# Performance work log

Measured on AMD Instinct MI355X. Metric: run time of the kernel, lower is better.

The kernel has to match this reference:

```python
import jax, jax.numpy as jnp
import numpy as np

N = 100000        # n_nodes (entities)
B = 1024          # batch of users
S = 32            # edge_threshold (sampled edges per node)
M = 64            # adj_matrix neighbors per node
D_IN = 64         # in_channel[0]
HID = 32          # out_channel[0] == in_channel[1]
D_OUT = 64        # out_channel[1]
K_STEP = 2
NUM_SAMPLE = 32
ITEM_LO, ITEM_HI = 0, 39999
SLOPE = 0.01      # leaky_relu default negative slope


def setup_inputs() -> dict:
    key = jax.random.key(0)
    ks = jax.random.split(key, 12)
    sc = lambda *sh: 1.0 / np.sqrt(sh[-1])
    return {
        "entity_embedding": jax.random.normal(ks[0], (N, D_IN), jnp.float32) * 0.1,
        "W1l": jax.random.normal(ks[1], (HID, D_IN), jnp.float32) * sc(HID, D_IN),
        "W1r": jax.random.normal(ks[2], (HID, D_IN), jnp.float32) * sc(HID, D_IN),
        "b1": jnp.zeros((HID,), jnp.float32),
        "W2l": jax.random.normal(ks[3], (D_OUT, HID), jnp.float32) * sc(D_OUT, HID),
        "W2r": jax.random.normal(ks[4], (D_OUT, HID), jnp.float32) * sc(D_OUT, HID),
        "b2": jnp.zeros((D_OUT,), jnp.float32),
        "disc_emb": jax.random.normal(ks[5], (N, D_OUT), jnp.float32) * 0.1,
        "users": jax.random.randint(ks[6], (B,), 0, ITEM_HI + 1, jnp.int32),
        "pos": jax.random.randint(ks[7], (B,), 0, ITEM_HI + 1, jnp.int32),
        "adj_matrix": jax.random.randint(ks[8], (N, M), 0, N, jnp.int32),
        "edge_matrix": jax.random.randint(ks[9], (N, S), 0, N, jnp.int32),
    }


def _leaky(x):
    return jnp.where(x >= 0, x, SLOPE * x)


def _sage(x, src, dst, Wl, Wr, b):
    # PyG SAGEConv: lin_l(mean_{j->i} x_j) + lin_r(x_i)
    sums = jax.ops.segment_sum(x[src], dst, num_segments=N)
    cnt = jax.ops.segment_sum(jnp.ones(src.shape, x.dtype), dst, num_segments=N)
    mean = sums / jnp.maximum(cnt, 1.0)[:, None]
    return mean @ Wl.T + b + x @ Wr.T


def _gcn(x, src, dst, W1l, W1r, b1, W2l, W2r, b2):
    h = _leaky(_sage(x, src, dst, W1l, W1r, b1))   # dropout = identity (eval)
    h = _sage(h, src, dst, W2l, W2r, b2)
    nrm = jnp.sqrt(jnp.sum(h * h, axis=1, keepdims=True))
    return h / jnp.maximum(nrm, 1e-12)             # F.normalize


def _kg_step(gcn, pos_idx, users, adj, explore_flag, step):
    u_e = gcn[users]                               # [B, d]
    pos_e = gcn[pos_idx]                           # [B, d]
    one_hop = adj[pos_idx] if explore_flag == 1 else adj[users]   # [B, M]
    i_e = gcn[one_hop]                             # [B, M, d]
    p = jnp.einsum('bmd,bd->bm', _leaky(pos_e[:, None, :] * i_e), u_e)
    logits = jax.nn.softmax(p, axis=1)
    if step == 1:
        nid = jnp.argmax(logits, axis=1)[:, None]
    else:
        _, nid = jax.lax.top_k(logits, NUM_SAMPLE)
    cand = jnp.take_along_axis(one_hop, nid, axis=1)
    prob = jnp.log(jnp.take_along_axis(logits, nid, axis=1))
    if step == 1:
        return cand[:, 0], prob[:, 0]
    return cand, prob


def _filter_entity(cand, key):
    rnd = jax.random.randint(key, cand.shape, ITEM_LO, ITEM_HI + 1, dtype=cand.dtype)
    bad = (cand > ITEM_HI) | (cand < ITEM_LO)
    return jnp.where(bad, rnd, cand)


def _prune_step(disc_emb, users, pos2, negs, logits):
    # stand-in for discriminator.item_rank (no_grad in original)
    u = jax.lax.stop_gradient(disc_emb[users])
    ranking = jnp.einsum('bd,bjd->bj', u,
                         jax.lax.stop_gradient(disc_emb[pos2] - disc_emb[negs]))
    idx = jnp.argmin(ranking, axis=1)[:, None]
    good_neg = jnp.take_along_axis(negs, idx, axis=1)[:, 0]
    good_logits = jnp.take_along_axis(logits, idx, axis=1)[:, 0]
    return good_neg, good_logits


def reference(entity_embedding, W1l, W1r, b1, W2l, W2r, b2, disc_emb,
              users, pos, adj_matrix, edge_matrix):
    src = jnp.repeat(jnp.arange(N, dtype=jnp.int32), S)   # build_edge node_index
    dst = edge_matrix.reshape(-1)
    gcn = _gcn(entity_embedding, src, dst, W1l, W1r, b1, W2l, W2r, b2)
    fkey = jax.random.key(123)
    neg_list, prob_list = [], []
    p = pos
    for k in range(K_STEP):
        one_hop, one_hop_logits = _kg_step(gcn, p, users, adj_matrix, 1, 1)
        cand, two_logits = _kg_step(gcn, one_hop, users, adj_matrix, 1, 2)
        cand = _filter_entity(cand, jax.random.fold_in(fkey, 2 * k))
        pos2, _ = _kg_step(gcn, p, users, adj_matrix, 2, 2)
        pos2 = _filter_entity(pos2, jax.random.fold_in(fkey, 2 * k + 1))
        good_neg, good_logits = _prune_step(disc_emb, users, pos2, cand, two_logits)
        good_logits = good_logits + one_hop_logits
        neg_list.append(good_neg)
        prob_list.append(good_logits)
        p = good_neg
    return jnp.stack(neg_list), jnp.stack(prob_list)
```

## Files before the change

### kernel.cpp

```cpp
#include <hip/hip_runtime.h>
#include <hip/hip_bf16.h>

#define N_NODES 100000
#define N_EDGES (N_NODES * 32)
#define BATCH   1024
#define SPAN    40000u
#define MULT    7296u
#define FILL_B  (N_EDGES / 256)

#define NB_BKT 391
#define EPB    4096
#define SBLK   782
#define BKT_CAP 8960


__host__ __device__ inline void threefry2x32(unsigned k0, unsigned k1,
                                             unsigned x0, unsigned x1,
                                             unsigned* o0, unsigned* o1)
{
  unsigned ks2 = k0 ^ k1 ^ 0x1BD11BDAu;
  unsigned v0 = x0 + k0, v1 = x1 + k1;
#define RL(x,d) (((x) << (d)) | ((x) >> (32 - (d))))
#define G4(a,b,c,dd) \
  v0 += v1; v1 = RL(v1,a);  v1 ^= v0; \
  v0 += v1; v1 = RL(v1,b);  v1 ^= v0; \
  v0 += v1; v1 = RL(v1,c);  v1 ^= v0; \
  v0 += v1; v1 = RL(v1,dd); v1 ^= v0;
  G4(13,15,26,6)  v0 += k1;  v1 += ks2 + 1u;
  G4(17,29,16,24) v0 += ks2; v1 += k0 + 2u;
  G4(13,15,26,6)  v0 += k0;  v1 += k1 + 3u;
  G4(17,29,16,24) v0 += k1;  v1 += ks2 + 4u;
  G4(13,15,26,6)  v0 += ks2; v1 += k0 + 5u;
#undef G4
#undef RL
  *o0 = v0; *o1 = v1;
}

__device__ __forceinline__ float bcastf(float v, int l)
{
  return __int_as_float(__builtin_amdgcn_readlane(__float_as_int(v), l));
}


__global__ void k_init_buckets(int* __restrict__ bbase, int* __restrict__ bcur)
{
  int i = blockIdx.x * 256 + threadIdx.x;
  if (i < NB_BKT) { bbase[i] = i * BKT_CAP; bcur[i] = i * BKT_CAP; }
}

__global__ __launch_bounds__(256) void k_bucket_hist(
    const int* __restrict__ edge, int* __restrict__ bhist)
{
  __shared__ int h[NB_BKT];
  for (int i = threadIdx.x; i < NB_BKT; i += 256) h[i] = 0;
  __syncthreads();
  int base = blockIdx.x * EPB;
  int cnt = N_EDGES - base; if (cnt > EPB) cnt = EPB;
  const int4* e4 = (const int4*)(edge + base);
  int nq = cnt >> 2;
  for (int i = threadIdx.x; i < nq; i += 256) {
    int4 v = e4[i];
    atomicAdd(&h[v.x >> 8], 1); atomicAdd(&h[v.y >> 8], 1);
    atomicAdd(&h[v.z >> 8], 1); atomicAdd(&h[v.w >> 8], 1);
  }
  __syncthreads();
  for (int i = threadIdx.x; i < NB_BKT; i += 256)
    if (h[i]) atomicAdd(&bhist[i], h[i]);
}

__global__ void k_scan_buckets(const int* __restrict__ bhist,
                               int* __restrict__ bbase, int* __restrict__ bcur)
{
  __shared__ int s[512];
  int t = threadIdx.x;
  s[t] = (t < NB_BKT) ? bhist[t] : 0;
  __syncthreads();
  for (int o = 1; o < 512; o <<= 1) {
    int u = (t >= o) ? s[t - o] : 0;
    __syncthreads();
    s[t] += u;
    __syncthreads();
  }
  if (t < NB_BKT) {
    int excl = s[t] - bhist[t];
    bbase[t] = excl;
    bcur[t]  = excl;
  }
}

__global__ __launch_bounds__(256) void k_bucket_scatter(
    const int* __restrict__ edge, int* __restrict__ bcur,
    int* __restrict__ pairs)
{
  __shared__ int  h[NB_BKT];
  __shared__ int  lbase[NB_BKT];
  __shared__ int  gbase[NB_BKT];
  __shared__ int  lcur[NB_BKT];
  __shared__ int2 buf[EPB];
  int t = threadIdx.x;
  for (int i = t; i < NB_BKT; i += 256) h[i] = 0;
  __syncthreads();
  int base = blockIdx.x * EPB;
  int cnt = N_EDGES - base; if (cnt > EPB) cnt = EPB;
  const int4* e4 = (const int4*)(edge + base);
  int nq = cnt >> 2;
  for (int i = t; i < nq; i += 256) {
    int4 v = e4[i];
    atomicAdd(&h[v.x >> 8], 1); atomicAdd(&h[v.y >> 8], 1);
    atomicAdd(&h[v.z >> 8], 1); atomicAdd(&h[v.w >> 8], 1);
  }
  __syncthreads();
  if (t < 64) {
    int run = 0;
    for (int c = 0; c < NB_BKT; c += 64) {
      int idx = c + t;
      int v = (idx < NB_BKT) ? h[idx] : 0;
      int orig = v;
      for (int o = 1; o < 64; o <<= 1) {
        int u = __shfl_up(v, o);
        if (t >= o) v += u;
      }
      if (idx < NB_BKT) lbase[idx] = run + v - orig;
      run += __shfl(v, 63);
    }
  }
  __syncthreads();
  for (int i = t; i < NB_BKT; i += 256) lcur[i] = lbase[i];
  __syncthreads();
  for (int i = t; i < nq; i += 256) {
    int4 v = e4[i];
    int eid = base + (i << 2);
    int p;
    p = atomicAdd(&lcur[v.x >> 8], 1); buf[p] = make_int2(v.x, (eid + 0) >> 5);
    p = atomicAdd(&lcur[v.y >> 8], 1); buf[p] = make_int2(v.y, (eid + 1) >> 5);
    p = atomicAdd(&lcur[v.z >> 8], 1); buf[p] = make_int2(v.z, (eid + 2) >> 5);
    p = atomicAdd(&lcur[v.w >> 8], 1); buf[p] = make_int2(v.w, (eid + 3) >> 5);
  }
  __syncthreads();
  for (int i = t; i < NB_BKT; i += 256) {
    int c = lcur[i] - lbase[i];
    gbase[i] = (c > 0) ? atomicAdd(&bcur[i], c) : 0;
  }
  __syncthreads();
  for (int i = t; i < cnt; i += 256) {
    int2 pr = buf[i];
    int b = pr.x >> 8;
    pairs[gbase[b] + (i - lbase[b])] = (pr.y << 8) | (pr.x & 255);
  }
}

__global__ __launch_bounds__(256) void k_bucket_csr(
    const int* __restrict__ bbase, const int* __restrict__ bcur,
    const int* __restrict__ pairs, int* __restrict__ csr,
    int* __restrict__ rowp, int* __restrict__ deg)
{
  __shared__ int nd[256], nb[256], nc[256];
  int b = blockIdx.x, t = threadIdx.x;
  int nb0 = b << 8;
  int ebase = bbase[b];
  int ecnt  = bcur[b] - ebase;
  nd[t] = 0; nc[t] = 0;
  __syncthreads();
  for (int i = t; i < ecnt; i += 256) {
    int pr = pairs[ebase + i];
    atomicAdd(&nd[pr & 255], 1);
  }
  __syncthreads();
  nb[t] = nd[t];
  __syncthreads();
  for (int o = 1; o < 256; o <<= 1) {
    int u = (t >= o) ? nb[t - o] : 0;
    __syncthreads();
    nb[t] += u;
    __syncthreads();
  }
  int excl = nb[t] - nd[t];
  int node = nb0 + t;
  if (node < N_NODES) { rowp[node] = ebase + excl; deg[node] = nd[t]; }
  __syncthreads();
  nb[t] = excl;
  __syncthreads();
  for (int i = t; i < ecnt; i += 256) {
    int pr = pairs[ebase + i];
    int l = pr & 255;
    int p = atomicAdd(&nc[l], 1);
    csr[ebase + nb[l] + p] = pr >> 8;
  }
}

__global__ __launch_bounds__(256) void k_gather_csr(
    const int* __restrict__ rowp, const int* __restrict__ deg,
    const int* __restrict__ csr, const float* __restrict__ src,
    float* __restrict__ out)
{
  int node = blockIdx.x * 8 + (threadIdx.x >> 5);
  int f = threadIdx.x & 31;
  int hb = threadIdx.x & 32;
  int sub = f >> 3;
  int q   = f & 7;
  int start = rowp[node];
  int dg = deg[node];
  const float4* src4 = (const float4*)src;
  float4 a0 = make_float4(0.f, 0.f, 0.f, 0.f);
  float4 a1 = make_float4(0.f, 0.f, 0.f, 0.f);
  for (int b0 = 0; b0 < dg; b0 += 32) {
    int idx = b0 + f;
    int e = (idx < dg) ? csr[start + idx] : -1;
#pragma unroll
    for (int j = 0; j < 8; j += 2) {
      int e0 = __shfl(e, hb + 4 * j + sub);
      int e1 = __shfl(e, hb + 4 * (j + 1) + sub);
      if (e0 >= 0) {
        float4 v = src4[(size_t)e0 * 8 + q];
        a0.x += v.x; a0.y += v.y; a0.z += v.z; a0.w += v.w;
      }
      if (e1 >= 0) {
        float4 v = src4[(size_t)e1 * 8 + q];
        a1.x += v.x; a1.y += v.y; a1.z += v.z; a1.w += v.w;
      }
    }
  }
  a0.x += a1.x; a0.y += a1.y; a0.z += a1.z; a0.w += a1.w;
  a0.x += __shfl_xor(a0.x, 8);  a0.y += __shfl_xor(a0.y, 8);
  a0.z += __shfl_xor(a0.z, 8);  a0.w += __shfl_xor(a0.w, 8);
  a0.x += __shfl_xor(a0.x, 16); a0.y += __shfl_xor(a0.y, 16);
  a0.z += __shfl_xor(a0.z, 16); a0.w += __shfl_xor(a0.w, 16);
  if (sub == 0) ((float4*)out)[(size_t)node * 8 + q] = a0;
}

__global__ __launch_bounds__(256) void k_fill_gemm(
    const int* __restrict__ edge, int* __restrict__ head, int* __restrict__ next,
    int nsub, const float* __restrict__ x, const float* __restrict__ W,
    float* __restrict__ y)
{
  __shared__ float sw[32 * 65];
  if (blockIdx.x < FILL_B) {
    int e = blockIdx.x * 256 + threadIdx.x;
    int d = edge[e];
    int sub = e & (nsub - 1);
    int old = atomicExch(head + sub * N_NODES + d, e);
    next[e] = old;
  } else {
    for (int t = threadIdx.x; t < 2048; t += 256) sw[(t >> 6) * 65 + (t & 63)] = W[t];
    __syncthreads();
    int i = (blockIdx.x - FILL_B) * 8 + (threadIdx.x >> 5);
    int f = threadIdx.x & 31;
    const float* xr = x + (size_t)i * 64;
    const float* wr = sw + f * 65;
    float acc = 0.f;
#pragma unroll
    for (int d = 0; d < 64; ++d) acc += xr[d] * wr[d];
    y[(size_t)i * 32 + f] = acc;
  }
}

template<int NSUB>
__global__ __launch_bounds__(256) void k_gather_ll(
    const int* __restrict__ head, const int* __restrict__ next,
    const float* __restrict__ src, float* __restrict__ out,
    int* __restrict__ deg_out)
{
  int node = blockIdx.x * 8 + (threadIdx.x >> 5);
  int f = threadIdx.x & 31;
  int hb = threadIdx.x & 32;
  int e = (f < NSUB) ? head[f * N_NODES + node] : -1;
  float acc = 0.f;
  int cnt = 0;
  while (true) {
    int es[NSUB];
    bool any = false;
#pragma unroll
    for (int j = 0; j < NSUB; ++j) { es[j] = __shfl(e, hb + j); any |= (es[j] != -1); }
    if (!any) break;
    int en = -1;
    if (f < NSUB && e != -1) en = next[e];
#pragma unroll
    for (int j = 0; j < NSUB; ++j)
      if (es[j] != -1) { acc += src[(size_t)(es[j] >> 5) * 32 + f]; cnt++; }
    e = en;
  }
  out[(size_t)node * 32 + f] = acc;
  if (deg_out != nullptr && f == 0) deg_out[node] = cnt;
}

#define DWB 1250
#define DNPW 20

__global__ __launch_bounds__(256) void k_gemm64x32(
    const float* __restrict__ x, const float* __restrict__ W, float* __restrict__ y)
{
  int lane = threadIdx.x & 63;
  int gw = blockIdx.x * 4 + (threadIdx.x >> 6);
  float wreg[64];
  const float* wrow = W + (size_t)(lane & 31) * 64;
#pragma unroll
  for (int d = 0; d < 64; ++d) wreg[d] = wrow[d];
  int n0 = gw * DNPW;
#pragma unroll 1
  for (int i = n0; i < n0 + DNPW; ++i) {
    float vin = x[(size_t)i * 64 + lane];
    float acc = 0.f;
#pragma unroll
    for (int d = 0; d < 64; ++d) acc += bcastf(vin, d) * wreg[d];
    if (lane < 32) y[(size_t)i * 32 + lane] = acc;
  }
}

__global__ __launch_bounds__(256) void k_scatter(
    const int* __restrict__ edge, const float* __restrict__ src,
    float* __restrict__ acc, int* __restrict__ cnt)
{
  int e = blockIdx.x * 8 + (threadIdx.x >> 5);
  int f = threadIdx.x & 31;
  int d = edge[e];
  atomicAdd(acc + (size_t)d * 32 + f, src[(size_t)(e >> 5) * 32 + f]);
  if (cnt != nullptr && f == 0) atomicAdd(cnt + d, 1);
}

__global__ __launch_bounds__(256) void k_layer1(
    const float* __restrict__ sum1, const int* __restrict__ cnt,
    const float* __restrict__ x, const float* __restrict__ W1r,
    const float* __restrict__ b1, float* __restrict__ h)
{
  int lane = threadIdx.x & 63;
  int gw = blockIdx.x * 4 + (threadIdx.x >> 6);
  float wreg[64];
  const float* wrow = W1r + (size_t)(lane & 31) * 64;
#pragma unroll
  for (int d = 0; d < 64; ++d) wreg[d] = wrow[d];
  float sb = b1[lane & 31];
  int n0 = gw * DNPW;
#pragma unroll 1
  for (int i = n0; i < n0 + DNPW; ++i) {
    float vin = x[(size_t)i * 64 + lane];
    float acc = 0.f;
#pragma unroll
    for (int d = 0; d < 64; ++d) acc += bcastf(vin, d) * wreg[d];
    if (lane < 32) {
      float c = fmaxf((float)cnt[i], 1.f);
      float mean = sum1[(size_t)i * 32 + lane] / c;
      float v = (mean + sb) + acc;
      h[(size_t)i * 32 + lane] = (v >= 0.f) ? v : 0.01f * v;
    }
  }
}

#define L2_BLOCKS 1250
#define L2_NPW    20
__global__ __launch_bounds__(256) void k_layer2(
    float* __restrict__ A, float* __restrict__ B, const int* __restrict__ cnt,
    const float* __restrict__ W2l, const float* __restrict__ W2r,
    const float* __restrict__ b2)
{
  int lane = threadIdx.x & 63;
  int gw = blockIdx.x * 4 + (threadIdx.x >> 6);
  float wl[32], wr[32];
#pragma unroll
  for (int f = 0; f < 32; ++f) { wl[f] = W2l[lane * 32 + f]; wr[f] = W2r[lane * 32 + f]; }
  float bb = b2[lane];
  int n0 = gw * L2_NPW;
#pragma unroll 1
  for (int i = n0; i < n0 + L2_NPW; ++i) {
    float c = fmaxf((float)cnt[i], 1.f);
    float vin;
    if (lane < 32) vin = B[(size_t)i * 32 + lane] / c;
    else           vin = A[(size_t)i * 32 + (lane - 32)];
    float acc = 0.f, acc2 = 0.f;
#pragma unroll
    for (int f = 0; f < 32; ++f) {
      acc  += bcastf(vin, f)      * wl[f];
      acc2 += bcastf(vin, 32 + f) * wr[f];
    }
    float t = (acc + bb) + acc2;
    float s = t * t;
#pragma unroll
    for (int o = 32; o > 0; o >>= 1) s += __shfl_xor(s, o);
    float g = t / fmaxf(sqrtf(s), 1e-12f);
    if (lane < 32) A[(size_t)i * 32 + lane]        = g;
    else           B[(size_t)i * 32 + (lane - 32)] = g;
  }
}


__device__ inline float kg_score_lds(const float* __restrict__ row,
                                     const float* sp, const float* su)
{
  float acc = 0.f;
#pragma unroll
  for (int d = 0; d < 64; ++d) {
    float t = sp[d] * row[d];
    t = (t >= 0.f) ? t : 0.01f * t;
    acc += t * su[d];
  }
  return acc;
}

__device__ inline float wave_softmax(float acc)
{
  float m = acc;
#pragma unroll
  for (int o = 32; o > 0; o >>= 1) m = fmaxf(m, __shfl_xor(m, o));
  float e = expf(acc - m);
  float Z = e;
#pragma unroll
  for (int o = 32; o > 0; o >>= 1) Z += __shfl_xor(Z, o);
  return e / Z;
}

__device__ inline void load_row(const float* glo, const float* ghi, int node,
                                int lane, float* smem)
{
  smem[lane] = (lane < 32) ? glo[(size_t)node * 32 + lane]
                           : ghi[(size_t)node * 32 + (lane - 32)];
}

__device__ inline void stage_rows(const float* __restrict__ glo,
                                  const float* __restrict__ ghi,
                                  int nb, int lane, float* sn)
{
#pragma unroll
  for (int j = 0; j < 64; ++j) {
    int rj = __builtin_amdgcn_readlane(nb, j);
    float v = (lane < 32) ? glo[(size_t)rj * 32 + lane]
                          : ghi[(size_t)rj * 32 + (lane - 32)];
    sn[j * 65 + lane] = v;
  }
}

__global__ __launch_bounds__(64) void k_kg_argmax(
    const float* __restrict__ glo, const float* __restrict__ ghi,
    const int* __restrict__ users, const int* __restrict__ pvec,
    const int* __restrict__ adj, int* __restrict__ sel_out,
    float* __restrict__ logit_out)
{
  int b = blockIdx.x, lane = threadIdx.x;
  int u = users[b], pb = pvec[b];
  __shared__ float su[64], sp[64];
  __shared__ float sn[64 * 65];
  load_row(glo, ghi, u,  lane, su);
  load_row(glo, ghi, pb, lane, sp);
  int nb = adj[(size_t)pb * 64 + lane];
  stage_rows(glo, ghi, nb, lane, sn);
  __syncthreads();
  float sm = wave_softmax(kg_score_lds(sn + lane * 65, sp, su));
  float v = sm; int i = lane;
#pragma unroll
  for (int o = 32; o > 0; o >>= 1) {
    float ov = __shfl_xor(v, o); int oi = __shfl_xor(i, o);
    if (ov > v || (ov == v && oi < i)) { v = ov; i = oi; }
  }
  float smw = __shfl(sm, i);
  int sel = __shfl(nb, i);
  if (lane == 0) { sel_out[b] = sel; logit_out[b] = logf(smw); }
}

__global__ __launch_bounds__(64) void k_kg_topk2(
    const float* __restrict__ glo, const float* __restrict__ ghi,
    const int* __restrict__ users, const int* __restrict__ srcA,
    const int* __restrict__ pvecB, const int* __restrict__ adj,
    unsigned a1a, unsigned a1b, unsigned a2a, unsigned a2b,
    unsigned c1a, unsigned c1b, unsigned c2a, unsigned c2b,
    int* __restrict__ candA, float* __restrict__ logA, int* __restrict__ candB)
{
  int b = blockIdx.x & (BATCH - 1);
  int var = blockIdx.x >> 10;
  int lane = threadIdx.x;
  int u = users[b];
  int pidx = (var == 0) ? srcA[b] : pvecB[b];
  int nbr  = (var == 0) ? srcA[b] : u;
  unsigned k1a = (var == 0) ? a1a : c1a, k1b = (var == 0) ? a1b : c1b;
  unsigned k2a = (var == 0) ? a2a : c2a, k2b = (var == 0) ? a2b : c2b;
  int* cand_out = (var == 0) ? candA : candB;
  float* logit_out = (var == 0) ? logA : nullptr;

  __shared__ float su[64], sp[64];
  __shared__ float sn[64 * 65];
  load_row(glo, ghi, u,    lane, su);
  load_row(glo, ghi, pidx, lane, sp);
  int nb = adj[(size_t)nbr * 64 + lane];
  stage_rows(glo, ghi, nb, lane, sn);
  __syncthreads();
  float sm = wave_softmax(kg_score_lds(sn + lane * 65, sp, su));
  int r = 0;
#pragma unroll
  for (int j = 0; j < 64; ++j) {
    float sj = bcastf(sm, j);
    if (sj > sm || (sj == sm && j < lane)) ++r;
  }
  if (r < 32) {
    int cand = nb;
    if (logit_out != nullptr) logit_out[b * 32 + r] = logf(sm);
    unsigned j = (unsigned)(b * 32 + r);
    unsigned h0, h1, l0, l1;
    threefry2x32(k1a, k1b, 0u, j, &h0, &h1);
    threefry2x32(k2a, k2b, 0u, j, &l0, &l1);
    unsigned hi = h0 ^ h1, lo = l0 ^ l1;
    unsigned rnd = ((hi % SPAN) * MULT + (lo % SPAN)) % SPAN;
    if (cand > 39999 || cand < 0) cand = (int)rnd;
    cand_out[b * 32 + r] = cand;
  }
}

__global__ __launch_bounds__(64) void k_kg_prune(
    const float* __restrict__ disc, const int* __restrict__ users,
    const int* __restrict__ cand, const float* __restrict__ two_log,
    const int* __restrict__ pos2, const float* __restrict__ one_log,
    float* __restrict__ out, int k, int* __restrict__ p_next)
{
  int b = blockIdx.x, lane = threadIdx.x;
  __shared__ float su[64];
  __shared__ float sd[64 * 65];
  su[lane] = disc[(size_t)users[b] * 64 + lane];
  int pr = (lane < 32) ? pos2[b * 32 + lane] : cand[b * 32 + (lane - 32)];
#pragma unroll
  for (int j = 0; j < 64; ++j) {
    int rj = __builtin_amdgcn_readlane(pr, j);
    sd[j * 65 + lane] = disc[(size_t)rj * 64 + lane];
  }
  __syncthreads();
  float r = 1e30f;
  if (lane < 32) {
    const float* dp = sd + lane * 65;
    const float* dn = sd + (32 + lane) * 65;
    float acc = 0.f;
#pragma unroll
    for (int d = 0; d < 64; ++d) acc += su[d] * (dp[d] - dn[d]);
    r = acc;
  }
  float v = r; int i = lane;
#pragma unroll
  for (int o = 32; o > 0; o >>= 1) {
    float ov = __shfl_xor(v, o); int oi = __shfl_xor(i, o);
    if (ov < v || (ov == v && oi < i)) { v = ov; i = oi; }
  }
  if (lane == 0) {
    int gn = cand[b * 32 + i];
    float gl = two_log[b * 32 + i] + one_log[b];
    out[k * BATCH + b]             = (float)gn;
    out[2 * BATCH + k * BATCH + b] = gl;
    p_next[b] = gn;
  }
}

extern "C" void kernel_launch(void* const* d_in, const int* in_sizes, int n_in,
                              void* d_out, int out_size, void* d_ws, size_t ws_size,
                              hipStream_t stream)
{
  const float* x    = (const float*)d_in[0];
  const float* W1l  = (const float*)d_in[1];
  const float* W1r  = (const float*)d_in[2];
  const float* b1   = (const float*)d_in[3];
  const float* W2l  = (const float*)d_in[4];
  const float* W2r  = (const float*)d_in[5];
  const float* b2   = (const float*)d_in[6];
  const float* disc = (const float*)d_in[7];
  const int*   users= (const int*)d_in[8];
  const int*   pos  = (const int*)d_in[9];
  const int*   adj  = (const int*)d_in[10];
  const int*   edge = (const int*)d_in[11];
  float* out = (float*)d_out;

  char* w = (char*)d_ws;
  const size_t NEED_FIX = 42036480;
  const size_t NEED_CSR = 39617792;
  float *A, *B;
  char* bb;

  if (ws_size >= NEED_FIX) {
    int*  csr   = (int*)(w);
    int*  rowp  = (int*)(w + 14013440);
    int*  deg   = (int*)(w + 14413440);
    int*  bbase = (int*)(w + 14813440);
    int*  bcur  = (int*)(w + 14815488);
    int*  pairs = (int*)(w + 14817536);
    A = (float*)(w + 14817536);
    B = (float*)(w + 28830976);
    bb = w + 41630976;
    k_init_buckets<<<2, 256, 0, stream>>>(bbase, bcur);
    k_bucket_scatter<<<SBLK, 256, 0, stream>>>(edge, bcur, pairs);
    k_bucket_csr<<<NB_BKT, 256, 0, stream>>>(bbase, bcur, pairs, csr, rowp, deg);
    k_gemm64x32<<<DWB, 256, 0, stream>>>(x, W1l, A);
    k_gather_csr<<<N_NODES / 8, 256, 0, stream>>>(rowp, deg, csr, A, B);
    k_layer1<<<DWB, 256, 0, stream>>>(B, deg, x, W1r, b1, A);
    k_gather_csr<<<N_NODES / 8, 256, 0, stream>>>(rowp, deg, csr, A, B);
    k_layer2<<<L2_BLOCKS, 256, 0, stream>>>(A, B, deg, W2l, W2r, b2);
  } else if (ws_size >= NEED_CSR) {
    int*  csr   = (int*)(w);
    int*  rowp  = (int*)(w + 12800000);
    int*  deg   = (int*)(w + 13200000);
    int*  bhist = (int*)(w + 13600000);
    int*  bbase = (int*)(w + 13604096);
    int*  bcur  = (int*)(w + 13608192);
    int*  pairs = (int*)(w + 13612288);
    A = (float*)(w + 13612288);
    B = (float*)(w + 26412288);
    bb = w + 39212288;
    hipMemsetAsync(bhist, 0, 4096, stream);
    k_bucket_hist<<<SBLK, 256, 0, stream>>>(edge, bhist);
    k_scan_buckets<<<1, 512, 0, stream>>>(bhist, bbase, bcur);
    k_bucket_scatter<<<SBLK, 256, 0, stream>>>(edge, bcur, pairs);
    k_bucket_csr<<<NB_BKT, 256, 0, stream>>>(bbase, bcur, pairs, csr, rowp, deg);
    k_gemm64x32<<<DWB, 256, 0, stream>>>(x, W1l, A);
    k_gather_csr<<<N_NODES / 8, 256, 0, stream>>>(rowp, deg, csr, A, B);
    k_layer1<<<DWB, 256, 0, stream>>>(B, deg, x, W1r, b1, A);
    k_gather_csr<<<N_NODES / 8, 256, 0, stream>>>(rowp, deg, csr, A, B);
    k_layer2<<<L2_BLOCKS, 256, 0, stream>>>(A, B, deg, W2l, W2r, b2);
  } else {
    int* cnt = (int*)w;
    A = (float*)(w + 409600);
    B = (float*)(w + 13209600);
    bb = w + 26009600;
    hipMemsetAsync(cnt, 0, 400000, stream);
    hipMemsetAsync(B, 0, 12800000, stream);
    k_gemm64x32<<<DWB, 256, 0, stream>>>(x, W1l, A);
    k_scatter<<<N_EDGES / 8, 256, 0, stream>>>(edge, A, B, cnt);
    k_layer1<<<DWB, 256, 0, stream>>>(B, cnt, x, W1r, b1, A);
    hipMemsetAsync(B, 0, 12800000, stream);
    k_scatter<<<N_EDGES / 8, 256, 0, stream>>>(edge, A, B, nullptr);
    k_layer2<<<L2_BLOCKS, 256, 0, stream>>>(A, B, cnt, W2l, W2r, b2);
  }

  int*   p_cur       = (int*)(bb);
  int*   one_hop_sel = (int*)(bb + 4096);
  float* one_hop_log = (float*)(bb + 8192);
  int*   cand        = (int*)(bb + 12288);
  float* two_log     = (float*)(bb + 143360);
  int*   pos2        = (int*)(bb + 274432);

  for (int k = 0; k < 2; ++k) {
    unsigned f0, f1, a1a, a1b, a2a, a2b, c1a, c1b, c2a, c2b;
    threefry2x32(0u, 123u, 0u, (unsigned)(2 * k), &f0, &f1);
    threefry2x32(f0, f1, 0u, 0u, &a1a, &a1b);
    threefry2x32(f0, f1, 0u, 1u, &a2a, &a2b);
    threefry2x32(0u, 123u, 0u, (unsigned)(2 * k + 1), &f0, &f1);
    threefry2x32(f0, f1, 0u, 0u, &c1a, &c1b);
    threefry2x32(f0, f1, 0u, 1u, &c2a, &c2b);

    const int* pvec = (k == 0) ? pos : p_cur;
    k_kg_argmax<<<BATCH, 64, 0, stream>>>(A, B, users, pvec, adj, one_hop_sel, one_hop_log);
    k_kg_topk2<<<2 * BATCH, 64, 0, stream>>>(A, B, users, one_hop_sel, pvec, adj,
                                             a1a, a1b, a2a, a2b, c1a, c1b, c2a, c2b,
                                             cand, two_log, pos2);
    k_kg_prune<<<BATCH, 64, 0, stream>>>(disc, users, cand, two_log, pos2,
                                         one_hop_log, out, k, p_cur);
  }
}
```

Before: 456.4 us.

## Remap dense GEMM kernels to one node per lane with uniform weight loads

Rewrites the three dense per-node transforms (W1l projection, layer1 and layer2) so each lane owns one node and accumulates all outputs in registers. Weights are read as wave-uniform float4 loads instead of readlane broadcasts, and the grid is sized to 391 blocks. The aim is to remove the readlane/broadcast overhead and the half-idle lanes of the old wave-per-node scheme. In exchange each lane reads its node row as strided float4 (uncoalesced across lanes) and register pressure rises; an asm barrier fixes the reduction order in layer2's norm.

```diff
diff --git a/kernel.cpp b/kernel.cpp
--- a/kernel.cpp
+++ b/kernel.cpp
@@ -41,6 +41,12 @@
   return __int_as_float(__builtin_amdgcn_readlane(__float_as_int(v), l));
 }
 
+__device__ __forceinline__ float fbar(float v)
+{
+  asm volatile("" : "+v"(v));
+  return v;
+}
+
 
 __global__ void k_init_buckets(int* __restrict__ bbase, int* __restrict__ bcur)
 {
@@ -283,26 +289,37 @@
   if (deg_out != nullptr && f == 0) deg_out[node] = cnt;
 }
 
-#define DWB 1250
-#define DNPW 20
-
-__global__ __launch_bounds__(256) void k_gemm64x32(
+#define DGB 391
+
+__global__ __launch_bounds__(256, 4) void k_gemm64x32(
     const float* __restrict__ x, const float* __restrict__ W, float* __restrict__ y)
 {
   int lane = threadIdx.x & 63;
-  int gw = blockIdx.x * 4 + (threadIdx.x >> 6);
-  float wreg[64];
-  const float* wrow = W + (size_t)(lane & 31) * 64;
-#pragma unroll
-  for (int d = 0; d < 64; ++d) wreg[d] = wrow[d];
-  int n0 = gw * DNPW;
+  int wv = blockIdx.x * 4 + (threadIdx.x >> 6);
+  int node = wv * 64 + lane;
+  bool ok = node < N_NODES;
+  const float4* x4 = (const float4*)(x + (size_t)node * 64);
+  const float4* W4 = (const float4*)W;
+  float acc[32];
+#pragma unroll
+  for (int o = 0; o < 32; ++o) acc[o] = 0.f;
 #pragma unroll 1
-  for (int i = n0; i < n0 + DNPW; ++i) {
-    float vin = x[(size_t)i * 64 + lane];
-    float acc = 0.f;
-#pragma unroll
-    for (int d = 0; d < 64; ++d) acc += bcastf(vin, d) * wreg[d];
-    if (lane < 32) y[(size_t)i * 32 + lane] = acc;
+  for (int j = 0; j < 16; ++j) {
+    float4 xv = ok ? x4[j] : make_float4(0.f, 0.f, 0.f, 0.f);
+#pragma unroll
+    for (int o = 0; o < 32; ++o) {
+      float4 wv4 = W4[o * 16 + j];
+      acc[o] += wv4.x * xv.x;
+      acc[o] += wv4.y * xv.y;
+      acc[o] += wv4.z * xv.z;
+      acc[o] += wv4.w * xv.w;
+    }
+  }
+  if (ok) {
+    float4* y4 = (float4*)(y + (size_t)node * 32);
+#pragma unroll
+    for (int k = 0; k < 8; ++k)
+      y4[k] = make_float4(acc[4 * k], acc[4 * k + 1], acc[4 * k + 2], acc[4 * k + 3]);
   }
 }
 
@@ -317,67 +334,141 @@
   if (cnt != nullptr && f == 0) atomicAdd(cnt + d, 1);
 }
 
-__global__ __launch_bounds__(256) void k_layer1(
+__global__ __launch_bounds__(256, 4) void k_layer1(
     const float* __restrict__ sum1, const int* __restrict__ cnt,
     const float* __restrict__ x, const float* __restrict__ W1r,
     const float* __restrict__ b1, float* __restrict__ h)
 {
   int lane = threadIdx.x & 63;
-  int gw = blockIdx.x * 4 + (threadIdx.x >> 6);
-  float wreg[64];
-  const float* wrow = W1r + (size_t)(lane & 31) * 64;
-#pragma unroll
-  for (int d = 0; d < 64; ++d) wreg[d] = wrow[d];
-  float sb = b1[lane & 31];
-  int n0 = gw * DNPW;
+  int wv = blockIdx.x * 4 + (threadIdx.x >> 6);
+  int node = wv * 64 + lane;
+  bool ok = node < N_NODES;
+  const float4* x4 = (const float4*)(x + (size_t)node * 64);
+  const float4* W4 = (const float4*)W1r;
+  float acc[32];
+#pragma unroll
+  for (int o = 0; o < 32; ++o) acc[o] = 0.f;
 #pragma unroll 1
-  for (int i = n0; i < n0 + DNPW; ++i) {
-    float vin = x[(size_t)i * 64 + lane];
-    float acc = 0.f;
-#pragma unroll
-    for (int d = 0; d < 64; ++d) acc += bcastf(vin, d) * wreg[d];
-    if (lane < 32) {
-      float c = fmaxf((float)cnt[i], 1.f);
-      float mean = sum1[(size_t)i * 32 + lane] / c;
-      float v = (mean + sb) + acc;
-      h[(size_t)i * 32 + lane] = (v >= 0.f) ? v : 0.01f * v;
+  for (int j = 0; j < 16; ++j) {
+    float4 xv = ok ? x4[j] : make_float4(0.f, 0.f, 0.f, 0.f);
+#pragma unroll
+    for (int o = 0; o < 32; ++o) {
+      float4 wv4 = W4[o * 16 + j];
+      acc[o] += wv4.x * xv.x;
+      acc[o] += wv4.y * xv.y;
+      acc[o] += wv4.z * xv.z;
+      acc[o] += wv4.w * xv.w;
     }
   }
-}
-
-#define L2_BLOCKS 1250
-#define L2_NPW    20
-__global__ __launch_bounds__(256) void k_layer2(
+  if (ok) {
+    float c = fmaxf((float)cnt[node], 1.f);
+    const float4* s4 = (const float4*)(sum1 + (size_t)node * 32);
+    float4* h4 = (float4*)(h + (size_t)node * 32);
+#pragma unroll
+    for (int k = 0; k < 8; ++k) {
+      float4 sv = s4[k];
+      float4 r;
+      r.x = ((sv.x / c) + b1[4 * k + 0]) + acc[4 * k + 0];
+      r.y = ((sv.y / c) + b1[4 * k + 1]) + acc[4 * k + 1];
+      r.z = ((sv.z / c) + b1[4 * k + 2]) + acc[4 * k + 2];
+      r.w = ((sv.w / c) + b1[4 * k + 3]) + acc[4 * k + 3];
+      r.x = (r.x >= 0.f) ? r.x : 0.01f * r.x;
+      r.y = (r.y >= 0.f) ? r.y : 0.01f * r.y;
+      r.z = (r.z >= 0.f) ? r.z : 0.01f * r.z;
+      r.w = (r.w >= 0.f) ? r.w : 0.01f * r.w;
+      h4[k] = r;
+    }
+  }
+}
+
+__device__ __forceinline__ void l2_half(
+    const float4* B4, const float4* A4, const float4* Wl4, const float4* Wr4,
+    const float* b2, float c, bool ok, int obase, float* t)
+{
+  float accA[32];
+#pragma unroll
+  for (int o = 0; o < 32; ++o) accA[o] = 0.f;
+#pragma unroll 1
+  for (int j = 0; j < 8; ++j) {
+    float4 bv = ok ? B4[j] : make_float4(0.f, 0.f, 0.f, 0.f);
+    bv.x /= c; bv.y /= c; bv.z /= c; bv.w /= c;
+#pragma unroll
+    for (int o = 0; o < 32; ++o) {
+      float4 w = Wl4[(obase + o) * 8 + j];
+      accA[o] += w.x * bv.x;
+      accA[o] += w.y * bv.y;
+      accA[o] += w.z * bv.z;
+      accA[o] += w.w * bv.w;
+    }
+  }
+#pragma unroll
+  for (int o = 0; o < 32; ++o) accA[o] = accA[o] + b2[obase + o];
+  float accB[32];
+#pragma unroll
+  for (int o = 0; o < 32; ++o) accB[o] = 0.f;
+#pragma unroll 1
+  for (int j = 0; j < 8; ++j) {
+    float4 av = ok ? A4[j] : make_float4(0.f, 0.f, 0.f, 0.f);
+#pragma unroll
+    for (int o = 0; o < 32; ++o) {
+      float4 w = Wr4[(obase + o) * 8 + j];
+      accB[o] += w.x * av.x;
+      accB[o] += w.y * av.y;
+      accB[o] += w.z * av.z;
+      accB[o] += w.w * av.w;
+    }
+  }
+#pragma unroll
+  for (int o = 0; o < 32; ++o) t[o] = accA[o] + accB[o];
+}
+
+__global__ __launch_bounds__(256, 4) void k_layer2(
     float* __restrict__ A, float* __restrict__ B, const int* __restrict__ cnt,
     const float* __restrict__ W2l, const float* __restrict__ W2r,
     const float* __restrict__ b2)
 {
   int lane = threadIdx.x & 63;
-  int gw = blockIdx.x * 4 + (threadIdx.x >> 6);
-  float wl[32], wr[32];
-#pragma unroll
-  for (int f = 0; f < 32; ++f) { wl[f] = W2l[lane * 32 + f]; wr[f] = W2r[lane * 32 + f]; }
-  float bb = b2[lane];
-  int n0 = gw * L2_NPW;
-#pragma unroll 1
-  for (int i = n0; i < n0 + L2_NPW; ++i) {
-    float c = fmaxf((float)cnt[i], 1.f);
-    float vin;
-    if (lane < 32) vin = B[(size_t)i * 32 + lane] / c;
-    else           vin = A[(size_t)i * 32 + (lane - 32)];
-    float acc = 0.f, acc2 = 0.f;
-#pragma unroll
-    for (int f = 0; f < 32; ++f) {
-      acc  += bcastf(vin, f)      * wl[f];
-      acc2 += bcastf(vin, 32 + f) * wr[f];
+  int wv = blockIdx.x * 4 + (threadIdx.x >> 6);
+  int node = wv * 64 + lane;
+  bool ok = node < N_NODES;
+  float c = 1.f;
+  if (ok) c = fmaxf((float)cnt[node], 1.f);
+  const float4* B4 = (const float4*)(B + (size_t)node * 32);
+  const float4* A4 = (const float4*)(A + (size_t)node * 32);
+  const float4* Wl4 = (const float4*)W2l;
+  const float4* Wr4 = (const float4*)W2r;
+  float t0[32], t1[32];
+  l2_half(B4, A4, Wl4, Wr4, b2, c, ok, 0,  t0);
+  l2_half(B4, A4, Wl4, Wr4, b2, c, ok, 32, t1);
+  float a[32];
+#pragma unroll
+  for (int k = 0; k < 32; ++k) {
+    float v0 = fbar(t0[k] * t0[k]);
+    float v1 = fbar(t1[k] * t1[k]);
+    a[k] = v0 + v1;
+  }
+  float bv[16];
+#pragma unroll
+  for (int k = 0; k < 16; ++k) bv[k] = a[k] + a[k + 16];
+  float cv[8];
+#pragma unroll
+  for (int k = 0; k < 8; ++k) cv[k] = bv[k] + bv[k + 8];
+  float dv[4];
+#pragma unroll
+  for (int k = 0; k < 4; ++k) dv[k] = cv[k] + cv[k + 4];
+  float ev0 = dv[0] + dv[2], ev1 = dv[1] + dv[3];
+  float s = (ev0 + ev1);
+  float den = fmaxf(sqrtf(s), 1e-12f);
+  if (ok) {
+    float4* Ao = (float4*)(A + (size_t)node * 32);
+    float4* Bo = (float4*)(B + (size_t)node * 32);
+#pragma unroll
+    for (int k = 0; k < 8; ++k) {
+      Ao[k] = make_float4(t0[4 * k] / den, t0[4 * k + 1] / den,
+                          t0[4 * k + 2] / den, t0[4 * k + 3] / den);
+      Bo[k] = make_float4(t1[4 * k] / den, t1[4 * k + 1] / den,
+                          t1[4 * k + 2] / den, t1[4 * k + 3] / den);
     }
-    float t = (acc + bb) + acc2;
-    float s = t * t;
-#pragma unroll
-    for (int o = 32; o > 0; o >>= 1) s += __shfl_xor(s, o);
-    float g = t / fmaxf(sqrtf(s), 1e-12f);
-    if (lane < 32) A[(size_t)i * 32 + lane]        = g;
-    else           B[(size_t)i * 32 + (lane - 32)] = g;
   }
 }
 
@@ -579,11 +670,11 @@
     k_init_buckets<<<2, 256, 0, stream>>>(bbase, bcur);
     k_bucket_scatter<<<SBLK, 256, 0, stream>>>(edge, bcur, pairs);
     k_bucket_csr<<<NB_BKT, 256, 0, stream>>>(bbase, bcur, pairs, csr, rowp, deg);
-    k_gemm64x32<<<DWB, 256, 0, stream>>>(x, W1l, A);
+    k_gemm64x32<<<DGB, 256, 0, stream>>>(x, W1l, A);
     k_gather_csr<<<N_NODES / 8, 256, 0, stream>>>(rowp, deg, csr, A, B);
-    k_layer1<<<DWB, 256, 0, stream>>>(B, deg, x, W1r, b1, A);
+    k_layer1<<<DGB, 256, 0, stream>>>(B, deg, x, W1r, b1, A);
     k_gather_csr<<<N_NODES / 8, 256, 0, stream>>>(rowp, deg, csr, A, B);
-    k_layer2<<<L2_BLOCKS, 256, 0, stream>>>(A, B, deg, W2l, W2r, b2);
+    k_layer2<<<DGB, 256, 0, stream>>>(A, B, deg, W2l, W2r, b2);
   } else if (ws_size >= NEED_CSR) {
     int*  csr   = (int*)(w);
     int*  rowp  = (int*)(w + 12800000);
@@ -600,11 +691,11 @@
     k_scan_buckets<<<1, 512, 0, stream>>>(bhist, bbase, bcur);
     k_bucket_scatter<<<SBLK, 256, 0, stream>>>(edge, bcur, pairs);
     k_bucket_csr<<<NB_BKT, 256, 0, stream>>>(bbase, bcur, pairs, csr, rowp, deg);
-    k_gemm64x32<<<DWB, 256, 0, stream>>>(x, W1l, A);
+    k_gemm64x32<<<DGB, 256, 0, stream>>>(x, W1l, A);
     k_gather_csr<<<N_NODES / 8, 256, 0, stream>>>(rowp, deg, csr, A, B);
-    k_layer1<<<DWB, 256, 0, stream>>>(B, deg, x, W1r, b1, A);
+    k_layer1<<<DGB, 256, 0, stream>>>(B, deg, x, W1r, b1, A);
     k_gather_csr<<<N_NODES / 8, 256, 0, stream>>>(rowp, deg, csr, A, B);
-    k_layer2<<<L2_BLOCKS, 256, 0, stream>>>(A, B, deg, W2l, W2r, b2);
+    k_layer2<<<DGB, 256, 0, stream>>>(A, B, deg, W2l, W2r, b2);
   } else {
     int* cnt = (int*)w;
     A = (float*)(w + 409600);
@@ -612,12 +703,12 @@
     bb = w + 26009600;
     hipMemsetAsync(cnt, 0, 400000, stream);
     hipMemsetAsync(B, 0, 12800000, stream);
-    k_gemm64x32<<<DWB, 256, 0, stream>>>(x, W1l, A);
+    k_gemm64x32<<<DGB, 256, 0, stream>>>(x, W1l, A);
     k_scatter<<<N_EDGES / 8, 256, 0, stream>>>(edge, A, B, cnt);
-    k_layer1<<<DWB, 256, 0, stream>>>(B, cnt, x, W1r, b1, A);
+    k_layer1<<<DGB, 256, 0, stream>>>(B, cnt, x, W1r, b1, A);
     hipMemsetAsync(B, 0, 12800000, stream);
     k_scatter<<<N_EDGES / 8, 256, 0, stream>>>(edge, A, B, nullptr);
-    k_layer2<<<L2_BLOCKS, 256, 0, stream>>>(A, B, cnt, W2l, W2r, b2);
+    k_layer2<<<DGB, 256, 0, stream>>>(A, B, cnt, W2l, W2r, b2);
   }
 
   int*   p_cur       = (int*)(bb);
```

After: 444.6 us. 1.03x faster.

## Map one node per lane in 64x32 GEMM and layer1 kernels

Applied to the files above, without the earlier changes.

Reworks the dense x@W kernels so each lane owns a whole node and accumulates all 32 outputs in registers. Input rows are read as float4 and weights are read as wave-uniform float4 loads that hit cache, replacing the cross-lane broadcast shuffles and the half-idle lanes of the old scheme. The risk is per-lane strided row loads (256 B stride), which coalesce poorly, plus higher register pressure from 32 accumulators.

```diff
diff --git a/kernel.cpp b/kernel.cpp
--- a/kernel.cpp
+++ b/kernel.cpp
@@ -283,26 +283,37 @@
   if (deg_out != nullptr && f == 0) deg_out[node] = cnt;
 }
 
-#define DWB 1250
-#define DNPW 20
-
-__global__ __launch_bounds__(256) void k_gemm64x32(
+#define DGB 391
+
+__global__ __launch_bounds__(256, 4) void k_gemm64x32(
     const float* __restrict__ x, const float* __restrict__ W, float* __restrict__ y)
 {
   int lane = threadIdx.x & 63;
-  int gw = blockIdx.x * 4 + (threadIdx.x >> 6);
-  float wreg[64];
-  const float* wrow = W + (size_t)(lane & 31) * 64;
-#pragma unroll
-  for (int d = 0; d < 64; ++d) wreg[d] = wrow[d];
-  int n0 = gw * DNPW;
+  int wv = blockIdx.x * 4 + (threadIdx.x >> 6);
+  int node = wv * 64 + lane;
+  bool ok = node < N_NODES;
+  const float4* x4 = (const float4*)(x + (size_t)node * 64);
+  const float4* W4 = (const float4*)W;
+  float acc[32];
+#pragma unroll
+  for (int o = 0; o < 32; ++o) acc[o] = 0.f;
 #pragma unroll 1
-  for (int i = n0; i < n0 + DNPW; ++i) {
-    float vin = x[(size_t)i * 64 + lane];
-    float acc = 0.f;
-#pragma unroll
-    for (int d = 0; d < 64; ++d) acc += bcastf(vin, d) * wreg[d];
-    if (lane < 32) y[(size_t)i * 32 + lane] = acc;
+  for (int j = 0; j < 16; ++j) {
+    float4 xv = ok ? x4[j] : make_float4(0.f, 0.f, 0.f, 0.f);
+#pragma unroll
+    for (int o = 0; o < 32; ++o) {
+      float4 wv4 = W4[o * 16 + j];
+      acc[o] += wv4.x * xv.x;
+      acc[o] += wv4.y * xv.y;
+      acc[o] += wv4.z * xv.z;
+      acc[o] += wv4.w * xv.w;
+    }
+  }
+  if (ok) {
+    float4* y4 = (float4*)(y + (size_t)node * 32);
+#pragma unroll
+    for (int k = 0; k < 8; ++k)
+      y4[k] = make_float4(acc[4 * k], acc[4 * k + 1], acc[4 * k + 2], acc[4 * k + 3]);
   }
 }
 
@@ -317,30 +328,49 @@
   if (cnt != nullptr && f == 0) atomicAdd(cnt + d, 1);
 }
 
-__global__ __launch_bounds__(256) void k_layer1(
+__global__ __launch_bounds__(256, 4) void k_layer1(
     const float* __restrict__ sum1, const int* __restrict__ cnt,
     const float* __restrict__ x, const float* __restrict__ W1r,
     const float* __restrict__ b1, float* __restrict__ h)
 {
   int lane = threadIdx.x & 63;
-  int gw = blockIdx.x * 4 + (threadIdx.x >> 6);
-  float wreg[64];
-  const float* wrow = W1r + (size_t)(lane & 31) * 64;
-#pragma unroll
-  for (int d = 0; d < 64; ++d) wreg[d] = wrow[d];
-  float sb = b1[lane & 31];
-  int n0 = gw * DNPW;
+  int wv = blockIdx.x * 4 + (threadIdx.x >> 6);
+  int node = wv * 64 + lane;
+  bool ok = node < N_NODES;
+  const float4* x4 = (const float4*)(x + (size_t)node * 64);
+  const float4* W4 = (const float4*)W1r;
+  float acc[32];
+#pragma unroll
+  for (int o = 0; o < 32; ++o) acc[o] = 0.f;
 #pragma unroll 1
-  for (int i = n0; i < n0 + DNPW; ++i) {
-    float vin = x[(size_t)i * 64 + lane];
-    float acc = 0.f;
-#pragma unroll
-    for (int d = 0; d < 64; ++d) acc += bcastf(vin, d) * wreg[d];
-    if (lane < 32) {
-      float c = fmaxf((float)cnt[i], 1.f);
-      float mean = sum1[(size_t)i * 32 + lane] / c;
-      float v = (mean + sb) + acc;
-      h[(size_t)i * 32 + lane] = (v >= 0.f) ? v : 0.01f * v;
+  for (int j = 0; j < 16; ++j) {
+    float4 xv = ok ? x4[j] : make_float4(0.f, 0.f, 0.f, 0.f);
+#pragma unroll
+    for (int o = 0; o < 32; ++o) {
+      float4 wv4 = W4[o * 16 + j];
+      acc[o] += wv4.x * xv.x;
+      acc[o] += wv4.y * xv.y;
+      acc[o] += wv4.z * xv.z;
+      acc[o] += wv4.w * xv.w;
+    }
+  }
+  if (ok) {
+    float c = fmaxf((float)cnt[node], 1.f);
+    const float4* s4 = (const float4*)(sum1 + (size_t)node * 32);
+    float4* h4 = (float4*)(h + (size_t)node * 32);
+#pragma unroll
+    for (int k = 0; k < 8; ++k) {
+      float4 sv = s4[k];
+      float4 r;
+      r.x = ((sv.x / c) + b1[4 * k + 0]) + acc[4 * k + 0];
+      r.y = ((sv.y / c) + b1[4 * k + 1]) + acc[4 * k + 1];
+      r.z = ((sv.z / c) + b1[4 * k + 2]) + acc[4 * k + 2];
+      r.w = ((sv.w / c) + b1[4 * k + 3]) + acc[4 * k + 3];
+      r.x = (r.x >= 0.f) ? r.x : 0.01f * r.x;
+      r.y = (r.y >= 0.f) ? r.y : 0.01f * r.y;
+      r.z = (r.z >= 0.f) ? r.z : 0.01f * r.z;
+      r.w = (r.w >= 0.f) ? r.w : 0.01f * r.w;
+      h4[k] = r;
     }
   }
 }
@@ -579,9 +609,9 @@
     k_init_buckets<<<2, 256, 0, stream>>>(bbase, bcur);
     k_bucket_scatter<<<SBLK, 256, 0, stream>>>(edge, bcur, pairs);
     k_bucket_csr<<<NB_BKT, 256, 0, stream>>>(bbase, bcur, pairs, csr, rowp, deg);
-    k_gemm64x32<<<DWB, 256, 0, stream>>>(x, W1l, A);
+    k_gemm64x32<<<DGB, 256, 0, stream>>>(x, W1l, A);
     k_gather_csr<<<N_NODES / 8, 256, 0, stream>>>(rowp, deg, csr, A, B);
-    k_layer1<<<DWB, 256, 0, stream>>>(B, deg, x, W1r, b1, A);
+    k_layer1<<<DGB, 256, 0, stream>>>(B, deg, x, W1r, b1, A);
     k_gather_csr<<<N_NODES / 8, 256, 0, stream>>>(rowp, deg, csr, A, B);
     k_layer2<<<L2_BLOCKS, 256, 0, stream>>>(A, B, deg, W2l, W2r, b2);
   } else if (ws_size >= NEED_CSR) {
@@ -600,9 +630,9 @@
     k_scan_buckets<<<1, 512, 0, stream>>>(bhist, bbase, bcur);
     k_bucket_scatter<<<SBLK, 256, 0, stream>>>(edge, bcur, pairs);
     k_bucket_csr<<<NB_BKT, 256, 0, stream>>>(bbase, bcur, pairs, csr, rowp, deg);
-    k_gemm64x32<<<DWB, 256, 0, stream>>>(x, W1l, A);
+    k_gemm64x32<<<DGB, 256, 0, stream>>>(x, W1l, A);
     k_gather_csr<<<N_NODES / 8, 256, 0, stream>>>(rowp, deg, csr, A, B);
-    k_layer1<<<DWB, 256, 0, stream>>>(B, deg, x, W1r, b1, A);
+    k_layer1<<<DGB, 256, 0, stream>>>(B, deg, x, W1r, b1, A);
     k_gather_csr<<<N_NODES / 8, 256, 0, stream>>>(rowp, deg, csr, A, B);
     k_layer2<<<L2_BLOCKS, 256, 0, stream>>>(A, B, deg, W2l, W2r, b2);
   } else {
@@ -612,9 +642,9 @@
     bb = w + 26009600;
     hipMemsetAsync(cnt, 0, 400000, stream);
     hipMemsetAsync(B, 0, 12800000, stream);
-    k_gemm64x32<<<DWB, 256, 0, stream>>>(x, W1l, A);
+    k_gemm64x32<<<DGB, 256, 0, stream>>>(x, W1l, A);
     k_scatter<<<N_EDGES / 8, 256, 0, stream>>>(edge, A, B, cnt);
-    k_layer1<<<DWB, 256, 0, stream>>>(B, cnt, x, W1r, b1, A);
+    k_layer1<<<DGB, 256, 0, stream>>>(B, cnt, x, W1r, b1, A);
     hipMemsetAsync(B, 0, 12800000, stream);
     k_scatter<<<N_EDGES / 8, 256, 0, stream>>>(edge, A, B, nullptr);
     k_layer2<<<L2_BLOCKS, 256, 0, stream>>>(A, B, cnt, W2l, W2r, b2);
```

Result: faster. 440.8 us (-3.4%).
